# Optimization experiments

Hardware: AMD Instinct MI355X
Metric: run time of the kernel (lower is better)

The kernel has to match this reference:

```python
import jax, jax.numpy as jnp
import numpy as np

# mode=1 coefficients from MSeE.__init__
A_COEFFS = jnp.array([1.0, -1.31861375911, 0.32059452332], dtype=jnp.float32)
B_COEFFS = jnp.array([0.95616638497, -1.31960414122, 0.36343775625], dtype=jnp.float32)


def _lfilter(x, a, b, clamp):
    """Direct-form-II-transposed-equivalent IIR filter, zero initial state.
    x: [B, T]; a, b: [3] with a[0] the normalizer. Matches torchaudio.functional.lfilter.
    """
    a = a / a[0]
    b = b / a[0] if False else b / A_COEFFS[0]  # a[0]==1 here; keep explicit normalization
    a_n = a
    b_n = b
    B_, T = x.shape
    # FIR numerator: fir[n] = b0*x[n] + b1*x[n-1] + b2*x[n-2] (zero-padded past)
    xp = jnp.pad(x, ((0, 0), (2, 0)))
    fir = b_n[0] * xp[:, 2:] + b_n[1] * xp[:, 1:-1] + b_n[2] * xp[:, :-2]  # [B, T]

    # IIR denominator recursion: y[n] = fir[n] - a1*y[n-1] - a2*y[n-2]
    def step(carry, f_t):
        y1, y2 = carry
        y = f_t - a_n[1] * y1 - a_n[2] * y2
        return (y, y1), y

    init = (jnp.zeros((B_,), x.dtype), jnp.zeros((B_,), x.dtype))
    _, ys = jax.lax.scan(step, init, fir.T)  # scan over time: ys [T, B]
    y = ys.T
    if clamp:
        y = jnp.clip(y, -1.0, 1.0)
    return y


def _filtfilt(x):
    # torchaudio.functional.filtfilt: forward lfilter (no clamp), flip, lfilter (clamp), flip
    fwd = _lfilter(x, A_COEFFS, B_COEFFS, clamp=False)
    bwd = _lfilter(jnp.flip(fwd, axis=-1), A_COEFFS, B_COEFFS, clamp=True)
    return jnp.flip(bwd, axis=-1)


def setup_inputs() -> dict:
    key = jax.random.key(0)
    k1, k2 = jax.random.split(key)
    B, T = 256, 65536
    predictions = jax.random.normal(k1, (B, T), dtype=jnp.float32)
    targets = jax.random.normal(k2, (B, T), dtype=jnp.float32)
    return {"predictions": predictions, "targets": targets}


def reference(predictions, targets):
    p = _filtfilt(predictions)
    t = _filtfilt(targets)
    return jnp.mean((p - t) ** 2)
```

## Files before the change

kernel.cpp:

```cpp
#include <hip/hip_runtime.h>

#define BB 256
#define TT 65536
#define LL 64
#define CC (TT / LL)
#define CSH 10

#define P1f  ( 1.31861375911f)
#define P2f  (-0.32059452332f)
#define B0f  ( 0.95616638497f)
#define B1f  (-1.31960414122f)
#define B2f  ( 0.36343775625f)

__device__ __forceinline__ float stepf(float xc, float& x1, float& x2,
                                       float& y1, float& y2) {
    float fir = fmaf(B0f, xc, fmaf(B1f, x1, B2f * x2));
    float y   = fmaf(P1f, y1, fmaf(P2f, y2, fir));
    y2 = y1; y1 = y;
    x2 = x1; x1 = xc;
    return y;
}

__global__ __launch_bounds__(256) void k_fwd_states(const float* __restrict__ xp,
                                                    const float* __restrict__ xt,
                                                    float2* __restrict__ stl) {
    int tid = blockIdx.x * 256 + threadIdx.x;
    int c  = tid & (CC - 1);
    int rs = tid >> CSH;
    const float* x = (rs < BB ? xp : xt) + (long)(rs & (BB - 1)) * TT;
    long base = (long)c * LL;
    float x1 = 0.f, x2 = 0.f;
    if (c > 0) { x1 = x[base - 1]; x2 = x[base - 2]; }
    float y1 = 0.f, y2 = 0.f;
    const float4* xv = (const float4*)(x + base);
    #pragma unroll
    for (int i = 0; i < LL / 4; ++i) {
        float4 v = xv[i];
        stepf(v.x, x1, x2, y1, y2);
        stepf(v.y, x1, x2, y1, y2);
        stepf(v.z, x1, x2, y1, y2);
        stepf(v.w, x1, x2, y1, y2);
    }
    stl[tid] = make_float2(y1, y2);
}

__device__ __forceinline__ void Apow(double n, double* M) {
    const double a1 = -1.31861375911, a2 = 0.32059452332;
    double disc = sqrt(a1 * a1 - 4.0 * a2);
    double r1 = (-a1 + disc) * 0.5, r2 = (-a1 - disc) * 0.5;
    double inv = 1.0 / (r1 - r2);
    double p1a = pow(r1, n + 1.0), p2a = pow(r2, n + 1.0);
    double p1b = pow(r1, n),       p2b = pow(r2, n);
    double p1c = pow(r1, n - 1.0), p2c = pow(r2, n - 1.0);
    M[0] = (p1a - p2a) * inv;
    M[1] = -a2 * (p1b - p2b) * inv;
    M[2] = (p1b - p2b) * inv;
    M[3] = -a2 * (p1c - p2c) * inv;
}

__global__ __launch_bounds__(256) void k_chain(const float2* __restrict__ stl,
                                               float2* __restrict__ sti) {
    int lane = threadIdx.x & 63;
    int row  = blockIdx.x * 4 + (threadIdx.x >> 6);
    double A1[4]; Apow((double)LL, A1);
    const float2* d = stl + (long)row * CC + lane * 16;
    double v1 = 0.0, v2 = 0.0;
    #pragma unroll
    for (int i = 0; i < 16; ++i) {
        float2 di = d[i];
        double n1 = (double)di.x + A1[0] * v1 + A1[1] * v2;
        double n2 = (double)di.y + A1[2] * v1 + A1[3] * v2;
        v1 = n1; v2 = n2;
    }
    #pragma unroll
    for (int k = 1; k < 64; k <<= 1) {
        double Mk[4]; Apow((double)LL * 16.0 * (double)k, Mk);
        double p1 = __shfl_up(v1, k);
        double p2 = __shfl_up(v2, k);
        if (lane >= k) {
            v1 = v1 + Mk[0] * p1 + Mk[1] * p2;
            v2 = v2 + Mk[2] * p1 + Mk[3] * p2;
        }
    }
    double e1 = __shfl_up(v1, 1), e2 = __shfl_up(v2, 1);
    if (lane == 0) { e1 = 0.0; e2 = 0.0; }
    float2* o = sti + (long)row * CC + lane * 16;
    double s1 = e1, s2 = e2;
    #pragma unroll
    for (int i = 0; i < 16; ++i) {
        o[i] = make_float2((float)s1, (float)s2);
        float2 di = d[i];
        double n1 = (double)di.x + A1[0] * s1 + A1[1] * s2;
        double n2 = (double)di.y + A1[2] * s1 + A1[3] * s2;
        s1 = n1; s2 = n2;
    }
}

__device__ __forceinline__ void ztaps(const float* x, long nb, float2 sn,
                                      float& z1, float& z2) {
    float xa = x[nb], xb = x[nb + 1], xm1 = x[nb - 1], xm2 = x[nb - 2];
    float f0 = fmaf(B0f, xa, fmaf(B1f, xm1, B2f * xm2));
    f0 = fmaf(P1f, sn.x, fmaf(P2f, sn.y, f0));
    float f1 = fmaf(B0f, xb, fmaf(B1f, xa, B2f * xm1));
    f1 = fmaf(P1f, f0, fmaf(P2f, sn.x, f1));
    z1 = f0; z2 = f1;
}

__global__ __launch_bounds__(256) void k_bwd_states(const float* __restrict__ xp,
                                                    const float* __restrict__ xt,
                                                    const float2* __restrict__ sti_f,
                                                    float2* __restrict__ stl_b) {
    int tid = blockIdx.x * 256 + threadIdx.x;
    int c  = tid & (CC - 1);
    int rs = tid >> CSH;
    const float* x = (rs < BB ? xp : xt) + (long)(rs & (BB - 1)) * TT;
    int cf = CC - 1 - c;
    long base = (long)cf * LL;
    float2 sf = sti_f[(rs << CSH) + cf];
    float buf[LL];
    const float4* xv = (const float4*)(x + base);
    #pragma unroll
    for (int i = 0; i < LL / 4; ++i) {
        float4 v = xv[i];
        buf[4 * i] = v.x; buf[4 * i + 1] = v.y;
        buf[4 * i + 2] = v.z; buf[4 * i + 3] = v.w;
    }
    float x1 = 0.f, x2 = 0.f;
    if (cf > 0) { x1 = x[base - 1]; x2 = x[base - 2]; }
    float y1 = sf.x, y2 = sf.y;
    #pragma unroll
    for (int j = 0; j < LL; ++j)
        buf[j] = stepf(buf[j], x1, x2, y1, y2);
    float z1 = 0.f, z2 = 0.f;
    if (c > 0) {
        float2 sn = sti_f[(rs << CSH) + cf + 1];
        ztaps(x, base + LL, sn, z1, z2);
    }
    float w1 = 0.f, w2 = 0.f;
    #pragma unroll
    for (int j = LL - 1; j >= 0; --j)
        stepf(buf[j], z1, z2, w1, w2);
    stl_b[tid] = make_float2(w1, w2);
}

__global__ __launch_bounds__(256) void k_final(const float* __restrict__ xp,
                                               const float* __restrict__ xt,
                                               const float2* __restrict__ sti_f,
                                               const float2* __restrict__ sti_b,
                                               float* __restrict__ acc) {
    int tid = blockIdx.x * 256 + threadIdx.x;
    int c = tid & (CC - 1);
    int r = tid >> CSH;
    int cf = CC - 1 - c;
    long base = (long)cf * LL;

    float bufp[LL];
    {
        const float* x = xp + (long)r * TT;
        float2 sf = sti_f[(r << CSH) + cf];
        const float4* xv = (const float4*)(x + base);
        #pragma unroll
        for (int i = 0; i < LL / 4; ++i) {
            float4 v = xv[i];
            bufp[4 * i] = v.x; bufp[4 * i + 1] = v.y;
            bufp[4 * i + 2] = v.z; bufp[4 * i + 3] = v.w;
        }
        float x1 = 0.f, x2 = 0.f;
        if (cf > 0) { x1 = x[base - 1]; x2 = x[base - 2]; }
        float y1 = sf.x, y2 = sf.y;
        #pragma unroll
        for (int j = 0; j < LL; ++j)
            bufp[j] = stepf(bufp[j], x1, x2, y1, y2);
        float z1 = 0.f, z2 = 0.f;
        if (c > 0) {
            float2 sn = sti_f[(r << CSH) + cf + 1];
            ztaps(x, base + LL, sn, z1, z2);
        }
        float2 sb = sti_b[(r << CSH) + c];
        float w1 = sb.x, w2 = sb.y;
        #pragma unroll
        for (int j = LL - 1; j >= 0; --j) {
            float w = stepf(bufp[j], z1, z2, w1, w2);
            bufp[j] = fminf(fmaxf(w, -1.f), 1.f);
        }
    }
    float accl = 0.f;
    {
        const float* x = xt + (long)r * TT;
        int rt = BB + r;
        float2 sf = sti_f[(rt << CSH) + cf];
        float buft[LL];
        const float4* xv = (const float4*)(x + base);
        #pragma unroll
        for (int i = 0; i < LL / 4; ++i) {
            float4 v = xv[i];
            buft[4 * i] = v.x; buft[4 * i + 1] = v.y;
            buft[4 * i + 2] = v.z; buft[4 * i + 3] = v.w;
        }
        float x1 = 0.f, x2 = 0.f;
        if (cf > 0) { x1 = x[base - 1]; x2 = x[base - 2]; }
        float y1 = sf.x, y2 = sf.y;
        #pragma unroll
        for (int j = 0; j < LL; ++j)
            buft[j] = stepf(buft[j], x1, x2, y1, y2);
        float z1 = 0.f, z2 = 0.f;
        if (c > 0) {
            float2 sn = sti_f[(rt << CSH) + cf + 1];
            ztaps(x, base + LL, sn, z1, z2);
        }
        float2 sb = sti_b[(rt << CSH) + c];
        float w1 = sb.x, w2 = sb.y;
        #pragma unroll
        for (int j = LL - 1; j >= 0; --j) {
            float w = stepf(buft[j], z1, z2, w1, w2);
            float d = bufp[j] - fminf(fmaxf(w, -1.f), 1.f);
            accl = fmaf(d, d, accl);
        }
    }
    for (int off = 32; off > 0; off >>= 1) accl += __shfl_down(accl, off);
    __shared__ float wsum[4];
    if ((threadIdx.x & 63) == 0) wsum[threadIdx.x >> 6] = accl;
    __syncthreads();
    if (threadIdx.x == 0)
        atomicAdd(acc, wsum[0] + wsum[1] + wsum[2] + wsum[3]);
}

__global__ void k_finish(const float* __restrict__ acc, float* __restrict__ out) {
    out[0] = acc[0] * (1.0f / (float)((long)BB * TT));
}

extern "C" void kernel_launch(void* const* d_in, const int* in_sizes, int n_in,
                              void* d_out, int out_size, void* d_ws, size_t ws_size,
                              hipStream_t stream) {
    const float* xp = (const float*)d_in[0];
    const float* xt = (const float*)d_in[1];
    float* out = (float*)d_out;

    const size_t one_st = (size_t)2 * BB * CC * sizeof(float2);
    char* w = (char*)d_ws;
    float2* stlf = (float2*)w;                 w += one_st;
    float2* stif = (float2*)w;                 w += one_st;
    float2* stlb = (float2*)w;                 w += one_st;
    float2* stib = (float2*)w;                 w += one_st;
    float*  acc  = (float*)w;

    hipMemsetAsync(acc, 0, sizeof(float), stream);

    const int nA = 2 * BB * CC;
    k_fwd_states<<<nA / 256, 256, 0, stream>>>(xp, xt, stlf);
    k_chain<<<(2 * BB) / 4, 256, 0, stream>>>(stlf, stif);
    k_bwd_states<<<nA / 256, 256, 0, stream>>>(xp, xt, stif, stlb);
    k_chain<<<(2 * BB) / 4, 256, 0, stream>>>(stlb, stib);
    k_final<<<(BB * CC) / 256, 256, 0, stream>>>(xp, xt, stif, stib, acc);
    k_finish<<<1, 1, 0, stream>>>(acc, out);
}
```

Measured before the change: 236.0 us.

## Halve chunk length, pair signals across half-waves in final pass, chain in place

The chunk length drops from 64 to 32 samples, which doubles the number of parallel chunks and halves the per-thread register buffer. The final kernel now gives the predictions and targets signals to the two half-waves of a wavefront and forms the difference with a cross-lane shuffle, so each thread filters one signal instead of two. A factor of 0.5 corrects for each squared difference being summed twice. The chain kernel rewrites its state buffer in place, cutting the workspace from four state arrays to two, and the forward-states kernel loads the whole chunk into registers before the recursion. The cost is twice as many chunk states to write, scan and read back.

```diff
diff --git a/kernel.cpp b/kernel.cpp
--- a/kernel.cpp
+++ b/kernel.cpp
@@ -2,9 +2,9 @@
 
 #define BB 256
 #define TT 65536
-#define LL 64
+#define LL 32
 #define CC (TT / LL)
-#define CSH 10
+#define CSH 11
 
 #define P1f  ( 1.31861375911f)
 #define P2f  (-0.32059452332f)
@@ -29,18 +29,20 @@
     int rs = tid >> CSH;
     const float* x = (rs < BB ? xp : xt) + (long)(rs & (BB - 1)) * TT;
     long base = (long)c * LL;
+    float buf[LL];
+    const float4* xv = (const float4*)(x + base);
+    #pragma unroll
+    for (int i = 0; i < LL / 4; ++i) {
+        float4 v = xv[i];
+        buf[4 * i] = v.x; buf[4 * i + 1] = v.y;
+        buf[4 * i + 2] = v.z; buf[4 * i + 3] = v.w;
+    }
     float x1 = 0.f, x2 = 0.f;
     if (c > 0) { x1 = x[base - 1]; x2 = x[base - 2]; }
     float y1 = 0.f, y2 = 0.f;
-    const float4* xv = (const float4*)(x + base);
-    #pragma unroll
-    for (int i = 0; i < LL / 4; ++i) {
-        float4 v = xv[i];
-        stepf(v.x, x1, x2, y1, y2);
-        stepf(v.y, x1, x2, y1, y2);
-        stepf(v.z, x1, x2, y1, y2);
-        stepf(v.w, x1, x2, y1, y2);
-    }
+    #pragma unroll
+    for (int j = 0; j < LL; ++j)
+        stepf(buf[j], x1, x2, y1, y2);
     stl[tid] = make_float2(y1, y2);
 }
 
@@ -58,15 +60,14 @@
     M[3] = -a2 * (p1c - p2c) * inv;
 }
 
-__global__ __launch_bounds__(256) void k_chain(const float2* __restrict__ stl,
-                                               float2* __restrict__ sti) {
+__global__ __launch_bounds__(256) void k_chain(float2* __restrict__ buf) {
     int lane = threadIdx.x & 63;
     int row  = blockIdx.x * 4 + (threadIdx.x >> 6);
     double A1[4]; Apow((double)LL, A1);
-    const float2* d = stl + (long)row * CC + lane * 16;
+    float2* d = buf + (long)row * CC + lane * (CC / 64);
     double v1 = 0.0, v2 = 0.0;
     #pragma unroll
-    for (int i = 0; i < 16; ++i) {
+    for (int i = 0; i < CC / 64; ++i) {
         float2 di = d[i];
         double n1 = (double)di.x + A1[0] * v1 + A1[1] * v2;
         double n2 = (double)di.y + A1[2] * v1 + A1[3] * v2;
@@ -74,7 +75,7 @@
     }
     #pragma unroll
     for (int k = 1; k < 64; k <<= 1) {
-        double Mk[4]; Apow((double)LL * 16.0 * (double)k, Mk);
+        double Mk[4]; Apow((double)LL * (double)(CC / 64) * (double)k, Mk);
         double p1 = __shfl_up(v1, k);
         double p2 = __shfl_up(v2, k);
         if (lane >= k) {
@@ -84,12 +85,11 @@
     }
     double e1 = __shfl_up(v1, 1), e2 = __shfl_up(v2, 1);
     if (lane == 0) { e1 = 0.0; e2 = 0.0; }
-    float2* o = sti + (long)row * CC + lane * 16;
     double s1 = e1, s2 = e2;
     #pragma unroll
-    for (int i = 0; i < 16; ++i) {
-        o[i] = make_float2((float)s1, (float)s2);
+    for (int i = 0; i < CC / 64; ++i) {
         float2 di = d[i];
+        d[i] = make_float2((float)s1, (float)s2);
         double n1 = (double)di.x + A1[0] * s1 + A1[1] * s2;
         double n2 = (double)di.y + A1[2] * s1 + A1[3] * s2;
         s1 = n1; s2 = n2;
@@ -149,73 +149,47 @@
                                                const float2* __restrict__ sti_b,
                                                float* __restrict__ acc) {
     int tid = blockIdx.x * 256 + threadIdx.x;
-    int c = tid & (CC - 1);
-    int r = tid >> CSH;
+    int lane = threadIdx.x & 63;
+    int w = tid >> 6;
+    int item = (w << 5) + (lane & 31);
+    int sig = lane >> 5;
+    int c = item & (CC - 1);
+    int r = item >> CSH;
     int cf = CC - 1 - c;
     long base = (long)cf * LL;
-
-    float bufp[LL];
-    {
-        const float* x = xp + (long)r * TT;
-        float2 sf = sti_f[(r << CSH) + cf];
-        const float4* xv = (const float4*)(x + base);
-        #pragma unroll
-        for (int i = 0; i < LL / 4; ++i) {
-            float4 v = xv[i];
-            bufp[4 * i] = v.x; bufp[4 * i + 1] = v.y;
-            bufp[4 * i + 2] = v.z; bufp[4 * i + 3] = v.w;
-        }
-        float x1 = 0.f, x2 = 0.f;
-        if (cf > 0) { x1 = x[base - 1]; x2 = x[base - 2]; }
-        float y1 = sf.x, y2 = sf.y;
-        #pragma unroll
-        for (int j = 0; j < LL; ++j)
-            bufp[j] = stepf(bufp[j], x1, x2, y1, y2);
-        float z1 = 0.f, z2 = 0.f;
-        if (c > 0) {
-            float2 sn = sti_f[(r << CSH) + cf + 1];
-            ztaps(x, base + LL, sn, z1, z2);
-        }
-        float2 sb = sti_b[(r << CSH) + c];
-        float w1 = sb.x, w2 = sb.y;
-        #pragma unroll
-        for (int j = LL - 1; j >= 0; --j) {
-            float w = stepf(bufp[j], z1, z2, w1, w2);
-            bufp[j] = fminf(fmaxf(w, -1.f), 1.f);
-        }
-    }
+    const float* x = (sig ? xt : xp) + (long)r * TT;
+    int row = (sig ? BB + r : r);
+
+    float buf[LL];
+    const float4* xv = (const float4*)(x + base);
+    #pragma unroll
+    for (int i = 0; i < LL / 4; ++i) {
+        float4 v = xv[i];
+        buf[4 * i] = v.x; buf[4 * i + 1] = v.y;
+        buf[4 * i + 2] = v.z; buf[4 * i + 3] = v.w;
+    }
+    float2 sf = sti_f[((long)row << CSH) + cf];
+    float x1 = 0.f, x2 = 0.f;
+    if (cf > 0) { x1 = x[base - 1]; x2 = x[base - 2]; }
+    float y1 = sf.x, y2 = sf.y;
+    #pragma unroll
+    for (int j = 0; j < LL; ++j)
+        buf[j] = stepf(buf[j], x1, x2, y1, y2);
+    float z1 = 0.f, z2 = 0.f;
+    if (c > 0) {
+        float2 sn = sti_f[((long)row << CSH) + cf + 1];
+        ztaps(x, base + LL, sn, z1, z2);
+    }
+    float2 sb = sti_b[((long)row << CSH) + c];
+    float w1 = sb.x, w2 = sb.y;
     float accl = 0.f;
-    {
-        const float* x = xt + (long)r * TT;
-        int rt = BB + r;
-        float2 sf = sti_f[(rt << CSH) + cf];
-        float buft[LL];
-        const float4* xv = (const float4*)(x + base);
-        #pragma unroll
-        for (int i = 0; i < LL / 4; ++i) {
-            float4 v = xv[i];
-            buft[4 * i] = v.x; buft[4 * i + 1] = v.y;
-            buft[4 * i + 2] = v.z; buft[4 * i + 3] = v.w;
-        }
-        float x1 = 0.f, x2 = 0.f;
-        if (cf > 0) { x1 = x[base - 1]; x2 = x[base - 2]; }
-        float y1 = sf.x, y2 = sf.y;
-        #pragma unroll
-        for (int j = 0; j < LL; ++j)
-            buft[j] = stepf(buft[j], x1, x2, y1, y2);
-        float z1 = 0.f, z2 = 0.f;
-        if (c > 0) {
-            float2 sn = sti_f[(rt << CSH) + cf + 1];
-            ztaps(x, base + LL, sn, z1, z2);
-        }
-        float2 sb = sti_b[(rt << CSH) + c];
-        float w1 = sb.x, w2 = sb.y;
-        #pragma unroll
-        for (int j = LL - 1; j >= 0; --j) {
-            float w = stepf(buft[j], z1, z2, w1, w2);
-            float d = bufp[j] - fminf(fmaxf(w, -1.f), 1.f);
-            accl = fmaf(d, d, accl);
-        }
+    #pragma unroll
+    for (int j = LL - 1; j >= 0; --j) {
+        float wv = stepf(buf[j], z1, z2, w1, w2);
+        float cl = fminf(fmaxf(wv, -1.f), 1.f);
+        float other = __shfl_xor(cl, 32);
+        float d = cl - other;
+        accl = fmaf(d, d, accl);
     }
     for (int off = 32; off > 0; off >>= 1) accl += __shfl_down(accl, off);
     __shared__ float wsum[4];
@@ -226,7 +200,7 @@
 }
 
 __global__ void k_finish(const float* __restrict__ acc, float* __restrict__ out) {
-    out[0] = acc[0] * (1.0f / (float)((long)BB * TT));
+    out[0] = acc[0] * (0.5f / (float)((long)BB * TT));
 }
 
 extern "C" void kernel_launch(void* const* d_in, const int* in_sizes, int n_in,
@@ -238,19 +212,17 @@
 
     const size_t one_st = (size_t)2 * BB * CC * sizeof(float2);
     char* w = (char*)d_ws;
-    float2* stlf = (float2*)w;                 w += one_st;
-    float2* stif = (float2*)w;                 w += one_st;
-    float2* stlb = (float2*)w;                 w += one_st;
-    float2* stib = (float2*)w;                 w += one_st;
+    float2* S1 = (float2*)w;                 w += one_st;
+    float2* S2 = (float2*)w;                 w += one_st;
     float*  acc  = (float*)w;
 
     hipMemsetAsync(acc, 0, sizeof(float), stream);
 
     const int nA = 2 * BB * CC;
-    k_fwd_states<<<nA / 256, 256, 0, stream>>>(xp, xt, stlf);
-    k_chain<<<(2 * BB) / 4, 256, 0, stream>>>(stlf, stif);
-    k_bwd_states<<<nA / 256, 256, 0, stream>>>(xp, xt, stif, stlb);
-    k_chain<<<(2 * BB) / 4, 256, 0, stream>>>(stlb, stib);
-    k_final<<<(BB * CC) / 256, 256, 0, stream>>>(xp, xt, stif, stib, acc);
+    k_fwd_states<<<nA / 256, 256, 0, stream>>>(xp, xt, S1);
+    k_chain<<<(2 * BB) / 4, 256, 0, stream>>>(S1);
+    k_bwd_states<<<nA / 256, 256, 0, stream>>>(xp, xt, S1, S2);
+    k_chain<<<(2 * BB) / 4, 256, 0, stream>>>(S2);
+    k_final<<<nA / 256, 256, 0, stream>>>(xp, xt, S1, S2, acc);
     k_finish<<<1, 1, 0, stream>>>(acc, out);
 }
```

Result: slower. 263.1 us (+11.5%).
